# Optimization experiments

Measured on AMD Instinct MI355X. Metric: run time of the kernel, lower is better.

The kernel has to match this reference:

```python
import jax, jax.numpy as jnp
import numpy as np

B, T, E, H = 64, 256, 300, 512


def _linear_init(key, fan_in, shape):
    s = 1.0 / np.sqrt(fan_in)
    return jax.random.uniform(key, shape, jnp.float32, -s, s)


def setup_inputs() -> dict:
    key = jax.random.key(0)
    ks = jax.random.split(key, 8)
    x = jax.random.normal(ks[0], (B, T, E), jnp.float32)
    # Valid transition programs: half the batch left-branching (S S R S R ...),
    # half right-branching (S^T followed by R^(T-1)).
    left = np.zeros(2 * T - 1, np.int32)
    left[2::2] = 1
    right = np.concatenate([np.zeros(T, np.int32), np.ones(T - 1, np.int32)])
    trans = np.stack([left if b % 2 == 0 else right for b in range(B)], axis=1)  # [2T-1, B]
    return {
        "x": x,
        "transitions": jnp.asarray(trans),
        "W_x": _linear_init(ks[1], E, (E, H)),
        "b_x": _linear_init(ks[2], E, (H,)),
        "W_g": _linear_init(ks[3], E, (E, H)),
        "b_g": _linear_init(ks[4], E, (H,)),
        "W_r": _linear_init(ks[5], 2 * H, (2 * H, 5 * H)),
        "b_r": _linear_init(ks[6], 2 * H, (5 * H,)),
    }


def _nary_cell(hc_l, hc_r, W_r, b_r):
    # hc_* : [B, 2H] = concat(h, c)
    h_l, c_l = jnp.split(hc_l, 2, axis=-1)
    h_r, c_r = jnp.split(hc_r, 2, axis=-1)
    proj = jnp.concatenate([h_l, h_r], axis=-1) @ W_r + b_r  # [B, 5H]
    i, f_l, f_r, g, o = jnp.split(proj, 5, axis=-1)
    c = jax.nn.sigmoid(i) * jnp.tanh(g) + jax.nn.sigmoid(f_l) * c_l + jax.nn.sigmoid(f_r) * c_r
    h = jax.nn.sigmoid(o) * jnp.tanh(c)
    return jnp.concatenate([h, c], axis=-1)


def _forward(x, transitions, W_x, b_x, W_g, b_g, W_r, b_r):
    Bb, Tt, _ = x.shape
    Hh = W_x.shape[1]
    # Buffer projections (x assumed reversed; buffers popped from the end).
    c_buf = x @ W_x + b_x                                  # [B, T, H]
    h_buf = jax.nn.sigmoid(x @ W_g + b_g) * jnp.tanh(c_buf)
    buffers = jnp.concatenate([h_buf, c_buf], axis=-1)     # [B, T, 2H]

    bidx = jnp.arange(Bb)
    stack0 = jnp.zeros((Bb, Tt, 2 * Hh), x.dtype)          # fixed-size stack
    sp0 = jnp.zeros((Bb,), jnp.int32)                      # stack pointer
    bp0 = jnp.full((Bb,), Tt, jnp.int32)                   # buffer pointer (pop from end)

    def step(carry, trans_t):
        stack, sp, bp = carry
        is_shift = trans_t == 0                            # [B] bool
        shifted = buffers[bidx, jnp.maximum(bp - 1, 0)]    # [B, 2H]
        child_r = stack[bidx, jnp.maximum(sp - 1, 0)]
        child_l = stack[bidx, jnp.maximum(sp - 2, 0)]
        reduced = _nary_cell(child_l, child_r, W_r, b_r)
        new_elem = jnp.where(is_shift[:, None], shifted, reduced)
        new_sp = jnp.where(is_shift, sp + 1, sp - 1)
        new_bp = jnp.where(is_shift, bp - 1, bp)
        stack = stack.at[bidx, jnp.maximum(new_sp - 1, 0)].set(new_elem)
        return (stack, new_sp, new_bp), None

    (stack, sp, _), _ = jax.lax.scan(step, (stack0, sp0, bp0), transitions)
    hc_root = stack[bidx, jnp.maximum(sp - 1, 0)]          # [B, 2H]
    return hc_root[:, :Hh]                                  # root h states [B, H]


def reference(x, transitions, W_x, b_x, W_g, b_g, W_r, b_r):
    return _forward(x, transitions, W_x, b_x, W_g, b_g, W_r, b_r)
```

## Files before the change

kernel.cpp:

```cpp
#include <hip/hip_runtime.h>
#include <hip/hip_bf16.h>

#define Bb 64
#define Tt 256
#define Ee 300
#define Hh 512
#define NSTEP (2 * Tt - 1)
#define NNODE (Tt - 1)
#define N5H (5 * Hh)

#define NG 8
#define GBATCH 8
#define NBLK 32
#define JPB 16
#define NC 80
#define SYNC_INTS (16 + NG * 1024)

typedef __bf16 v8bf __attribute__((ext_vector_type(8)));
typedef float v4f __attribute__((ext_vector_type(4)));
typedef unsigned long long u64;
typedef unsigned int u32;
typedef unsigned char u8;

__device__ __forceinline__ float sigm(float x) { return 1.f / (1.f + __expf(-x)); }

__global__ __launch_bounds__(256) void leaf_kernel(
    const float* __restrict__ x, const float* __restrict__ Wx,
    const float* __restrict__ bx, const float* __restrict__ Wg,
    const float* __restrict__ bg,
    __hip_bfloat16* __restrict__ leaf_h, float* __restrict__ leaf_c)
{
    __shared__ __align__(16) float xs[16][304];
    const int tid = threadIdx.x;
    const int n = blockIdx.x * 256 + tid;
    const long r0 = (long)blockIdx.y * 16;

    for (int i = tid; i < 16 * Ee; i += 256) {
        int r = i / Ee, k = i - r * Ee;
        xs[r][k] = x[(r0 + r) * Ee + k];
    }
    __syncthreads();

    float accx[16], accg[16];
    const float bxv = bx[n], bgv = bg[n];
#pragma unroll
    for (int r = 0; r < 16; r++) { accx[r] = bxv; accg[r] = bgv; }

    for (int k = 0; k < Ee; k += 4) {
        float wx[4], wg[4];
#pragma unroll
        for (int u = 0; u < 4; u++) {
            wx[u] = Wx[(long)(k + u) * Hh + n];
            wg[u] = Wg[(long)(k + u) * Hh + n];
        }
#pragma unroll
        for (int r = 0; r < 16; r++) {
            const float4 xv = *(const float4*)&xs[r][k];
            accx[r] = fmaf(xv.x, wx[0], accx[r]);
            accx[r] = fmaf(xv.y, wx[1], accx[r]);
            accx[r] = fmaf(xv.z, wx[2], accx[r]);
            accx[r] = fmaf(xv.w, wx[3], accx[r]);
            accg[r] = fmaf(xv.x, wg[0], accg[r]);
            accg[r] = fmaf(xv.y, wg[1], accg[r]);
            accg[r] = fmaf(xv.z, wg[2], accg[r]);
            accg[r] = fmaf(xv.w, wg[3], accg[r]);
        }
    }
#pragma unroll
    for (int r = 0; r < 16; r++) {
        const float c = accx[r];
        const float h = sigm(accg[r]) * tanhf(c);
        const long idx = (r0 + r) * Hh + n;
        leaf_c[idx] = c;
        leaf_h[idx] = __float2bfloat16(h);
    }
}

__global__ __launch_bounds__(256) void wtr_kernel(const float* __restrict__ Wr,
                                                  __hip_bfloat16* __restrict__ WtG)
{
    __shared__ float ts[64][65];
    const int tid = threadIdx.x;
    const long g0 = (long)blockIdx.x * 64;
    const int k0 = (int)blockIdx.y * 64;
    const int r = tid >> 6;
    const int c = tid & 63;
    __bf16* Wo = (__bf16*)WtG;
#pragma unroll
    for (int i = 0; i < 16; i++)
        ts[r + i * 4][c] = Wr[(long)(k0 + r + i * 4) * N5H + g0 + c];
    __syncthreads();
#pragma unroll
    for (int i = 0; i < 16; i++)
        Wo[(g0 + r + i * 4) * 1024 + k0 + c] = (__bf16)ts[c][r + i * 4];
}

__global__ __launch_bounds__(64) void sched_kernel(
    const int* __restrict__ trans,
    int* __restrict__ node_l, int* __restrict__ node_r,
    int* __restrict__ root_src, int* __restrict__ offs,
    int* __restrict__ items, int* __restrict__ max_lv,
    int* __restrict__ sync)
{
    __shared__ short stck[Bb][Tt];
    __shared__ unsigned char lvl[Bb][NNODE];
    __shared__ unsigned char trans_s[NSTEP][Bb];
    __shared__ int counts[NG][256];
    __shared__ int offs_s[NG][257];
    __shared__ int maxl_s[NG];
    const int b = threadIdx.x;

    if (b < NG) maxl_s[b] = 0;
    for (int i4 = b; i4 < SYNC_INTS / 4; i4 += Bb)
        ((int4*)sync)[i4] = make_int4(0, 0, 0, 0);
    for (int i = b; i < NG * 256; i += Bb) counts[i >> 8][i & 255] = 0;
    for (int i4 = b; i4 < (NSTEP * Bb) / 4; i4 += Bb) {
        const int4 v = ((const int4*)trans)[i4];
        const int f = 4 * i4;
        trans_s[(f + 0) >> 6][(f + 0) & 63] = (unsigned char)v.x;
        trans_s[(f + 1) >> 6][(f + 1) & 63] = (unsigned char)v.y;
        trans_s[(f + 2) >> 6][(f + 2) & 63] = (unsigned char)v.z;
        trans_s[(f + 3) >> 6][(f + 3) & 63] = (unsigned char)v.w;
    }
    __syncthreads();

    int sp = 0, bp = Tt, nid = 0, maxl = 0;
    for (int t = 0; t < NSTEP; t++) {
        if (trans_s[t][b] == 0) {
            bp -= 1;
            stck[b][sp] = (short)bp; sp += 1;
        } else {
            const int rs = stck[b][sp - 1];
            const int ls = stck[b][sp - 2];
            const int l_lv = (ls < Tt) ? 0 : (int)lvl[b][ls - Tt];
            const int r_lv = (rs < Tt) ? 0 : (int)lvl[b][rs - Tt];
            const int le = 1 + (l_lv > r_lv ? l_lv : r_lv);
            lvl[b][nid] = (unsigned char)le;
            node_l[b * NNODE + nid] = (l_lv << 9) | ls;
            node_r[b * NNODE + nid] = (r_lv << 9) | rs;
            if (le > maxl) maxl = le;
            sp -= 2;
            stck[b][sp] = (short)(Tt + nid); sp += 1;
            nid += 1;
        }
    }
    root_src[b] = (int)stck[b][0];
    const int g = b >> 3;
    for (int i = 0; i < nid; i++) atomicAdd(&counts[g][lvl[b][i]], 1);
    atomicMax(&maxl_s[g], maxl);
    __syncthreads();
    if (b < NG) {
        int acc = 0;
        for (int l = 0; l < 256; l++) { offs_s[b][l] = acc; acc += counts[b][l]; }
        offs_s[b][256] = acc;
        max_lv[b] = maxl_s[b];
    }
    __syncthreads();
    for (int i = b; i < NG * 256; i += Bb) counts[i >> 8][i & 255] = offs_s[i >> 8][i & 255];
    __syncthreads();
    for (int i = 0; i < nid; i++) {
        const int pos = atomicAdd(&counts[g][lvl[b][i]], 1);
        items[g * (GBATCH * NNODE) + pos] = (b << 16) | i;
    }
    for (int i = b; i < NG * 257; i += Bb) offs[i] = offs_s[i / 257][i % 257];
}

__global__ __launch_bounds__(512) void tree_kernel(
    const __hip_bfloat16* __restrict__ WtG, const float* __restrict__ br,
    const __hip_bfloat16* __restrict__ leaf_h, const float* __restrict__ leaf_c,
    __hip_bfloat16* __restrict__ node_h, float* __restrict__ node_c,
    const int* __restrict__ node_l, const int* __restrict__ node_r,
    const int* __restrict__ root_src, const int* __restrict__ offs,
    const int* __restrict__ items, const int* __restrict__ max_lv,
    float* __restrict__ out, int* __restrict__ sync)
{
    __shared__ float Cs[8][8][84];
    __shared__ float Cred[8][84];
    __shared__ float brs[NC];
    __shared__ u32 mHL[2048], mHR[2048], mCL[2048], mCR[2048], mFL[2048];
    __shared__ u64 hPl[16], hPr[16], cPl[16], cPr[16];
    __shared__ int outm[16];
    __shared__ int s_info;
    __shared__ int force_pad[5120];

    const int tid = threadIdx.x;

    if (tid == 0) {
        int xcc;
        asm volatile("s_getreg_b32 %0, hwreg(HW_REG_XCC_ID)" : "=s"(xcc));
        xcc &= 7;
        const int rank = atomicAdd(&sync[2 + xcc], 1);
        __builtin_amdgcn_s_waitcnt(0);
        const int n = atomicAdd(&sync[0], 1);
        if (n == 255) {
            int ok = 1;
            for (int i = 0; i < 8; i++)
                ok &= (__hip_atomic_load(&sync[2 + i], __ATOMIC_RELAXED,
                                         __HIP_MEMORY_SCOPE_AGENT) == NBLK);
            __hip_atomic_store(&sync[1], ok ? 2 : 1, __ATOMIC_RELAXED,
                               __HIP_MEMORY_SCOPE_AGENT);
        }
        int m;
        while ((m = __hip_atomic_load(&sync[1], __ATOMIC_RELAXED,
                                      __HIP_MEMORY_SCOPE_AGENT)) == 0) {}
        const int grp_ = (m == 2) ? xcc : ((int)blockIdx.x >> 5);
        const int mem_ = (m == 2) ? rank : ((int)blockIdx.x & 31);
        s_info = (m << 16) | (grp_ << 8) | mem_;
    }
    __syncthreads();
    const int info0 = s_info;
    const bool l2m = (info0 >> 16) == 2;
    const int grp = (info0 >> 8) & 255;
    const int mem = info0 & 255;
    const int j0 = mem * JPB;

    const int* offsG = offs + grp * 257;
    const int* itemsG = items + grp * (GBATCH * NNODE);
    int* cntG = sync + 16 + grp * 1024;

    const int ML = max_lv[grp];
    if (ML < 0) { volatile int* fp = force_pad; fp[tid] = 1; }

    const int wave = tid >> 6;
    const int lane = tid & 63;
    const int quad = lane >> 4;
    const int l15 = lane & 15;
    const int kq = wave;

    u32* node_h32 = (u32*)node_h;
    const char* const hBaseL = (const char*)leaf_h;
    const char* const hBaseN = (const char*)node_h;
    const char* const cBaseL = (const char*)leaf_c;
    const char* const cBaseN = (const char*)node_c;

    v8bf wreg[5][4];
#pragma unroll
    for (int nt = 0; nt < 5; nt++) {
        const int c = nt * 16 + l15;
        const long gcol = (long)((c % 5) * Hh + j0 + c / 5);
#pragma unroll
        for (int t = 0; t < 4; t++)
            wreg[nt][t] = *(const v8bf*)&WtG[gcol * 1024 + kq * 128 + t * 32 + quad * 8];
    }
    if (tid < NC) brs[tid] = br[(tid % 5) * Hh + j0 + tid / 5];

    for (int idx = tid; idx < 255 * 8; idx += 512) {
        const int lev = 1 + (idx >> 3);
        const int m = idx & 7;
        u32 fl = 1u << 29;
        u32 hl = 0, hr = 0, cl = 0, cr = 0;
        if (lev <= ML) {
            const int s = offsG[lev], e = offsG[lev + 1];
            const int M = e - s;
            if (M > 0) {
                const int it = itemsG[s + (m < M ? m : 0)];
                const int b = it >> 16, nd = it & 0xffff;
                const int lraw = node_l[b * NNODE + nd];
                const int rraw = node_r[b * NNODE + nd];
                const int ls = lraw & 511, llv = lraw >> 9;
                const int rs = rraw & 511, rlv = rraw >> 9;
                hl = (ls < Tt) ? (u32)((b * Tt + ls) * Hh * 2)
                               : ((u32)((b * NNODE + (ls - Tt)) * Hh * 2) | 0x80000000u);
                cl = (ls < Tt) ? (u32)((b * Tt + ls) * Hh * 4)
                               : ((u32)((b * NNODE + (ls - Tt)) * Hh * 4) | 0x80000000u);
                hr = (rs < Tt) ? (u32)((b * Tt + rs) * Hh * 2)
                               : ((u32)((b * NNODE + (rs - Tt)) * Hh * 2) | 0x80000000u);
                cr = (rs < Tt) ? (u32)((b * Tt + rs) * Hh * 4)
                               : ((u32)((b * NNODE + (rs - Tt)) * Hh * 4) | 0x80000000u);
                fl = (u32)it & 0x07ffffffu;
                if (llv > 0 && llv == lev - 1) fl |= 1u << 27;
                if (rlv > 0 && rlv == lev - 1) fl |= 1u << 28;
                if (m >= M) fl |= 1u << 29;
                if (Tt + nd == root_src[b]) fl |= 1u << 30;
            }
        }
        mHL[8 + idx] = hl; mHR[8 + idx] = hr;
        mCL[8 + idx] = cl; mCR[8 + idx] = cr;
        mFL[8 + idx] = fl;
    }

    auto prep = [&](int base, int M, int plv) {
        if (lane < 16) {
            const int m = lane;
            const int it = itemsG[base + (m < M ? m : 0)];
            const int b = it >> 16;
            const int nd = it & 0xffff;
            const int lraw = node_l[b * NNODE + nd];
            const int rraw = node_r[b * NNODE + nd];
            const int ls = lraw & 511, llv = lraw >> 9;
            const int rs = rraw & 511, rlv = rraw >> 9;
            hPl[m] = (ls < Tt) ? (u64)(leaf_h + ((long)b * Tt + ls) * Hh)
                               : (u64)(node_h + ((long)b * NNODE + (ls - Tt)) * Hh);
            cPl[m] = (ls < Tt) ? (u64)(leaf_c + ((long)b * Tt + ls) * Hh)
                               : (u64)(node_c + ((long)b * NNODE + (ls - Tt)) * Hh);
            hPr[m] = (rs < Tt) ? (u64)(leaf_h + ((long)b * Tt + rs) * Hh)
                               : (u64)(node_h + ((long)b * NNODE + (rs - Tt)) * Hh);
            cPr[m] = (rs < Tt) ? (u64)(leaf_c + ((long)b * Tt + rs) * Hh)
                               : (u64)(node_c + ((long)b * NNODE + (rs - Tt)) * Hh);
            int fl = it;
            if (llv > 0 && llv == plv - 1) fl |= (1 << 27);
            if (rlv > 0 && rlv == plv - 1) fl |= (1 << 28);
            if (Tt + nd == root_src[b]) fl |= (1 << 30);
            if (m >= M) fl |= (1 << 29);
            outm[m] = fl;
        }
    };

    auto gate_store = [&](u32 fe, float clv0, float clv1, float crv0, float crv1) {
        const int jl2 = (lane & 7) * 2;
        if (!(fe & (1u << 29))) {
            const int b = (int)(fe >> 16) & 63;
            const int nd = (int)(fe & 0xffff);
            float cv[2], hv[2];
            const float clv[2] = {clv0, clv1};
            const float crv[2] = {crv0, crv1};
            const int mm = lane >> 3;
#pragma unroll
            for (int jj = 0; jj < 2; jj++) {
                const int jc = (jl2 + jj) * 5;
                const float iv = Cred[mm][jc + 0];
                const float fl = Cred[mm][jc + 1];
                const float fr = Cred[mm][jc + 2];
                const float gv = Cred[mm][jc + 3];
                const float ov = Cred[mm][jc + 4];
                cv[jj] = sigm(iv) * tanhf(gv) + sigm(fl) * clv[jj] + sigm(fr) * crv[jj];
                hv[jj] = sigm(ov) * tanhf(cv[jj]);
            }
            union { float f[2]; u64 u; } cp;
            cp.f[0] = cv[0]; cp.f[1] = cv[1];
            const __hip_bfloat16 h0 = __float2bfloat16(hv[0]);
            const __hip_bfloat16 h1 = __float2bfloat16(hv[1]);
            const u32 hpack = (u32)(*(const unsigned short*)&h0)
                            | ((u32)(*(const unsigned short*)&h1) << 16);
            u64* cdst = (u64*)(node_c + ((long)b * NNODE + nd) * Hh + j0 + jl2);
            u32* hdst = node_h32 + ((long)b * NNODE + nd) * (Hh / 2) + (j0 + jl2) / 2;
            if (l2m) {
                *cdst = cp.u;
                *hdst = hpack;
            } else {
                __hip_atomic_store(cdst, cp.u, __ATOMIC_RELAXED, __HIP_MEMORY_SCOPE_AGENT);
                __hip_atomic_store(hdst, hpack, __ATOMIC_RELAXED, __HIP_MEMORY_SCOPE_AGENT);
            }
            if (fe & (1u << 30)) {
                out[(long)b * Hh + j0 + jl2]     = hv[0];
                out[(long)b * Hh + j0 + jl2 + 1] = hv[1];
            }
        }
    };

    auto do_mfma = [&](v8bf a0, v8bf a1, v8bf a2, v8bf a3) {
        v8bf a[4] = {a0, a1, a2, a3};
#pragma unroll
        for (int nt = 0; nt < 5; nt++) {
            v4f acc = {0.f, 0.f, 0.f, 0.f};
#pragma unroll
            for (int t = 0; t < 4; t++)
                acc = __builtin_amdgcn_mfma_f32_16x16x32_bf16(a[t], wreg[nt][t], acc, 0, 0, 0);
            if (quad < 2) {
#pragma unroll
                for (int rg = 0; rg < 4; rg++)
                    Cs[kq][quad * 4 + rg][nt * 16 + l15] = acc[rg];
            }
        }
    };

    auto reduce = [&]() {
        for (int t = tid; t < 8 * NC; t += 512) {
            const int m = t / NC, c = t - m * NC;
            float r = brs[c];
#pragma unroll
            for (int w = 0; w < 8; w++) r += Cs[w][m][c];
            Cred[m][c] = r;
        }
    };

    __syncthreads();

    const int kb = (kq & 3) * 128 + quad * 8;

    for (int lev = 1; lev <= ML; lev++) {
        const int s = offsG[lev], e = offsG[lev + 1];
        const int mb = lev * 8;

        const int miA = mb + (l15 & 7);
        const u32 flA = mFL[miA];
        const bool hot = (flA >> (27 + (kq >> 2))) & 1;
        const u32 ho = (kq < 4) ? mHL[miA] : mHR[miA];
        const __hip_bfloat16* hp = (const __hip_bfloat16*)
            (((ho & 0x80000000u) ? hBaseN : hBaseL) + (ho & 0x7fffffffu));
        v8bf a0, a1, a2, a3;
        if (!hot) {
            a0 = *(const v8bf*)(hp + kb);
            a1 = *(const v8bf*)(hp + kb + 32);
            a2 = *(const v8bf*)(hp + kb + 64);
            a3 = *(const v8bf*)(hp + kb + 96);
        }
        float clv0 = 0.f, clv1 = 0.f, crv0 = 0.f, crv1 = 0.f;
        bool hotL = false, hotR = false;
        u32 fe = 0;
        const float* cpl = nullptr;
        const float* cpr = nullptr;
        if (wave == 0) {
            const int mi0 = mb + (lane >> 3);
            fe = mFL[mi0];
            hotL = (fe >> 27) & 1;
            hotR = (fe >> 28) & 1;
            const u32 ocl = mCL[mi0], ocr = mCR[mi0];
            cpl = (const float*)(((ocl & 0x80000000u) ? cBaseN : cBaseL) + (ocl & 0x7fffffffu));
            cpr = (const float*)(((ocr & 0x80000000u) ? cBaseN : cBaseL) + (ocr & 0x7fffffffu));
            const int jo = j0 + (lane & 7) * 2;
            if (!hotL) {
                union { u64 u; float f[2]; } t;
                t.u = *(const u64*)(cpl + jo);
                clv0 = t.f[0]; clv1 = t.f[1];
            }
            if (!hotR) {
                union { u64 u; float f[2]; } t;
                t.u = *(const u64*)(cpr + jo);
                crv0 = t.f[0]; crv1 = t.f[1];
            }
        }

        if (lev > 1 && wave == 0) {
            int* cw = cntG + (lev - 1) * 4;
            while (__hip_atomic_load(cw, __ATOMIC_RELAXED,
                                     __HIP_MEMORY_SCOPE_AGENT) < NBLK) {}
        }
        __syncthreads();

        if (hot) {
            a0 = *(const v8bf*)(hp + kb);
            a1 = *(const v8bf*)(hp + kb + 32);
            a2 = *(const v8bf*)(hp + kb + 64);
            a3 = *(const v8bf*)(hp + kb + 96);
        }
        if (wave == 0) {
            const int jo = j0 + (lane & 7) * 2;
            if (hotL) {
                union { u64 u; float f[2]; } t;
                t.u = *(const u64*)(cpl + jo);
                clv0 = t.f[0]; clv1 = t.f[1];
            }
            if (hotR) {
                union { u64 u; float f[2]; } t;
                t.u = *(const u64*)(cpr + jo);
                crv0 = t.f[0]; crv1 = t.f[1];
            }
        }
        do_mfma(a0, a1, a2, a3);
        __syncthreads();
        reduce();
        __syncthreads();
        if (wave == 0) gate_store(fe, clv0, clv1, crv0, crv1);

        for (int base = s + 8; base < e; base += 8) {
            __syncthreads();
            if (wave == 0) prep(base, (e - base < 8) ? (e - base) : 8, lev);
            __syncthreads();
            const __hip_bfloat16* hp2 =
                (const __hip_bfloat16*)((kq < 4) ? hPl[l15 & 7] : hPr[l15 & 7]);
            float xl0 = 0.f, xl1 = 0.f, xr0 = 0.f, xr1 = 0.f;
            u32 fe2 = 1u << 29;
            if (wave == 0) {
                fe2 = (u32)outm[lane >> 3];
                const int jo = j0 + (lane & 7) * 2;
                union { u64 u; float f[2]; } t;
                t.u = *(const u64*)((const float*)cPl[lane >> 3] + jo);
                xl0 = t.f[0]; xl1 = t.f[1];
                t.u = *(const u64*)((const float*)cPr[lane >> 3] + jo);
                xr0 = t.f[0]; xr1 = t.f[1];
            }
            do_mfma(*(const v8bf*)(hp2 + kb), *(const v8bf*)(hp2 + kb + 32),
                    *(const v8bf*)(hp2 + kb + 64), *(const v8bf*)(hp2 + kb + 96));
            __syncthreads();
            reduce();
            __syncthreads();
            if (wave == 0) gate_store(fe2, xl0, xl1, xr0, xr1);
        }

        if (wave == 0) {
            __builtin_amdgcn_s_waitcnt(0);
            if (lev < ML && lane == 0) atomicAdd(cntG + lev * 4, 1);
        }
        __syncthreads();
    }
}

extern "C" void kernel_launch(void* const* d_in, const int* in_sizes, int n_in,
                              void* d_out, int out_size, void* d_ws, size_t ws_size,
                              hipStream_t stream)
{
    const float* x   = (const float*)d_in[0];
    const int* trans = (const int*)d_in[1];
    const float* Wx  = (const float*)d_in[2];
    const float* bx  = (const float*)d_in[3];
    const float* Wg  = (const float*)d_in[4];
    const float* bg  = (const float*)d_in[5];
    const float* Wr  = (const float*)d_in[6];
    const float* br  = (const float*)d_in[7];
    float* out = (float*)d_out;

    char* p = (char*)d_ws;
    auto take = [&](size_t bytes) -> char* {
        char* r = p;
        p += (bytes + 255) & ~(size_t)255;
        return r;
    };
    __hip_bfloat16* leaf_h = (__hip_bfloat16*)take((size_t)Bb * Tt * Hh * 2);
    float* leaf_c          = (float*)take((size_t)Bb * Tt * Hh * 4);
    __hip_bfloat16* node_h = (__hip_bfloat16*)take((size_t)Bb * NNODE * Hh * 2);
    float* node_c          = (float*)take((size_t)Bb * NNODE * Hh * 4);
    int* node_l   = (int*)take((size_t)Bb * NNODE * 4);
    int* node_r   = (int*)take((size_t)Bb * NNODE * 4);
    int* root_src = (int*)take(Bb * 4);
    int* offs     = (int*)take((size_t)NG * 257 * 4);
    int* items    = (int*)take((size_t)NG * GBATCH * NNODE * 4);
    int* max_lv   = (int*)take(NG * 4);
    __hip_bfloat16* WtG = (__hip_bfloat16*)take((size_t)N5H * 1024 * 2);
    int* sync     = (int*)take((size_t)SYNC_INTS * 4);

    hipLaunchKernelGGL(leaf_kernel, dim3(Hh / 256, (Bb * Tt) / 16), dim3(256), 0, stream,
                       x, Wx, bx, Wg, bg, leaf_h, leaf_c);
    hipLaunchKernelGGL(wtr_kernel, dim3(N5H / 64, 1024 / 64), dim3(256), 0, stream,
                       Wr, WtG);
    hipLaunchKernelGGL(sched_kernel, dim3(1), dim3(64), 0, stream,
                       trans, node_l, node_r, root_src, offs, items, max_lv, sync);

    void* args[] = { (void*)&WtG, (void*)&br, (void*)&leaf_h, (void*)&leaf_c,
                     (void*)&node_h, (void*)&node_c, (void*)&node_l, (void*)&node_r,
                     (void*)&root_src, (void*)&offs, (void*)&items, (void*)&max_lv,
                     (void*)&out, (void*)&sync };
    hipLaunchCooperativeKernel((const void*)tree_kernel, dim3(256), dim3(512),
                               args, 0, stream);
}
```

Measured before the change: 1.260 ms.

## Compute leaf projections with split-bf16 MFMA instead of scalar FP32 FMAs

Replaces the scalar FP32 leaf projection kernel with an MFMA kernel. Both x and the weights are split into bf16 hi/lo parts, and three products (hi*hi, hi*lo, lo*hi) recover near-FP32 accuracy. A new pre-pass kernel transposes Wx/Wg into K-padded hi/lo bf16 buffers. The aim is to move the leaf GEMM onto matrix cores, at the cost of an extra weight-split pass and some precision loss from the dropped lo*lo term.

```diff
diff --git a/kernel.cpp b/kernel.cpp
--- a/kernel.cpp
+++ b/kernel.cpp
@@ -8,6 +8,7 @@
 #define NSTEP (2 * Tt - 1)
 #define NNODE (Tt - 1)
 #define N5H (5 * Hh)
+#define LK 320
 
 #define NG 8
 #define GBATCH 8
@@ -24,55 +25,101 @@
 
 __device__ __forceinline__ float sigm(float x) { return 1.f / (1.f + __expf(-x)); }
 
-__global__ __launch_bounds__(256) void leaf_kernel(
-    const float* __restrict__ x, const float* __restrict__ Wx,
-    const float* __restrict__ bx, const float* __restrict__ Wg,
+__global__ __launch_bounds__(256) void wsplit_kernel(
+    const float* __restrict__ Wx, const float* __restrict__ Wg,
+    __bf16* __restrict__ WxHi, __bf16* __restrict__ WxLo,
+    __bf16* __restrict__ WgHi, __bf16* __restrict__ WgLo)
+{
+    __shared__ float ts[64][65];
+    const int tid = threadIdx.x;
+    const int g0 = blockIdx.x * 64;
+    const int k0 = blockIdx.y * 64;
+    const float* W = blockIdx.z ? Wg : Wx;
+    __bf16* Hi = blockIdx.z ? WgHi : WxHi;
+    __bf16* Lo = blockIdx.z ? WgLo : WxLo;
+    const int r = tid >> 6, c = tid & 63;
+#pragma unroll
+    for (int i = 0; i < 16; i++) {
+        const int k = k0 + r + i * 4;
+        ts[r + i * 4][c] = (k < Ee) ? W[(long)k * Hh + g0 + c] : 0.f;
+    }
+    __syncthreads();
+#pragma unroll
+    for (int i = 0; i < 16; i++) {
+        const float v = ts[c][r + i * 4];
+        const __bf16 hi = (__bf16)v;
+        const __bf16 lo = (__bf16)(v - (float)hi);
+        const long o = (long)(g0 + r + i * 4) * LK + k0 + c;
+        Hi[o] = hi;
+        Lo[o] = lo;
+    }
+}
+
+__global__ __launch_bounds__(256) void leaf_mfma_kernel(
+    const float* __restrict__ x, const float* __restrict__ bx,
     const float* __restrict__ bg,
+    const __bf16* __restrict__ WxHi, const __bf16* __restrict__ WxLo,
+    const __bf16* __restrict__ WgHi, const __bf16* __restrict__ WgLo,
     __hip_bfloat16* __restrict__ leaf_h, float* __restrict__ leaf_c)
 {
-    __shared__ __align__(16) float xs[16][304];
     const int tid = threadIdx.x;
-    const int n = blockIdx.x * 256 + tid;
-    const long r0 = (long)blockIdx.y * 16;
-
-    for (int i = tid; i < 16 * Ee; i += 256) {
-        int r = i / Ee, k = i - r * Ee;
-        xs[r][k] = x[(r0 + r) * Ee + k];
-    }
-    __syncthreads();
-
-    float accx[16], accg[16];
-    const float bxv = bx[n], bgv = bg[n];
-#pragma unroll
-    for (int r = 0; r < 16; r++) { accx[r] = bxv; accg[r] = bgv; }
-
-    for (int k = 0; k < Ee; k += 4) {
-        float wx[4], wg[4];
-#pragma unroll
-        for (int u = 0; u < 4; u++) {
-            wx[u] = Wx[(long)(k + u) * Hh + n];
-            wg[u] = Wg[(long)(k + u) * Hh + n];
-        }
-#pragma unroll
-        for (int r = 0; r < 16; r++) {
-            const float4 xv = *(const float4*)&xs[r][k];
-            accx[r] = fmaf(xv.x, wx[0], accx[r]);
-            accx[r] = fmaf(xv.y, wx[1], accx[r]);
-            accx[r] = fmaf(xv.z, wx[2], accx[r]);
-            accx[r] = fmaf(xv.w, wx[3], accx[r]);
-            accg[r] = fmaf(xv.x, wg[0], accg[r]);
-            accg[r] = fmaf(xv.y, wg[1], accg[r]);
-            accg[r] = fmaf(xv.z, wg[2], accg[r]);
-            accg[r] = fmaf(xv.w, wg[3], accg[r]);
-        }
-    }
-#pragma unroll
-    for (int r = 0; r < 16; r++) {
-        const float c = accx[r];
-        const float h = sigm(accg[r]) * tanhf(c);
-        const long idx = (r0 + r) * Hh + n;
-        leaf_c[idx] = c;
-        leaf_h[idx] = __float2bfloat16(h);
+    const int wave = tid >> 6, lane = tid & 63;
+    const int quad = lane >> 4, l15 = lane & 15;
+    const long r0 = (long)blockIdx.x * 64 + wave * 16;
+    const float* xr = x + (r0 + l15) * Ee;
+
+    v8bf ahi[10], alo[10];
+#pragma unroll
+    for (int t = 0; t < 10; t++) {
+        float v[8];
+        if (t < 9) {
+            const float4 p0 = *(const float4*)&xr[t * 32 + quad * 8];
+            const float4 p1 = *(const float4*)&xr[t * 32 + quad * 8 + 4];
+            v[0] = p0.x; v[1] = p0.y; v[2] = p0.z; v[3] = p0.w;
+            v[4] = p1.x; v[5] = p1.y; v[6] = p1.z; v[7] = p1.w;
+        } else {
+#pragma unroll
+            for (int j = 0; j < 8; j++) {
+                const int k = 288 + quad * 8 + j;
+                v[j] = (k < Ee) ? xr[k] : 0.f;
+            }
+        }
+#pragma unroll
+        for (int j = 0; j < 8; j++) {
+            const __bf16 h = (__bf16)v[j];
+            ahi[t][j] = h;
+            alo[t][j] = (__bf16)(v[j] - (float)h);
+        }
+    }
+
+    for (int nt = 0; nt < 32; nt++) {
+        const int n0 = nt * 16;
+        const long cb = (long)(n0 + l15) * LK + quad * 8;
+        v4f ax = {0.f, 0.f, 0.f, 0.f}, ag = {0.f, 0.f, 0.f, 0.f};
+#pragma unroll
+        for (int t = 0; t < 10; t++) {
+            const v8bf wxh = *(const v8bf*)&WxHi[cb + t * 32];
+            const v8bf wxl = *(const v8bf*)&WxLo[cb + t * 32];
+            const v8bf wgh = *(const v8bf*)&WgHi[cb + t * 32];
+            const v8bf wgl = *(const v8bf*)&WgLo[cb + t * 32];
+            ax = __builtin_amdgcn_mfma_f32_16x16x32_bf16(ahi[t], wxh, ax, 0, 0, 0);
+            ag = __builtin_amdgcn_mfma_f32_16x16x32_bf16(ahi[t], wgh, ag, 0, 0, 0);
+            ax = __builtin_amdgcn_mfma_f32_16x16x32_bf16(ahi[t], wxl, ax, 0, 0, 0);
+            ag = __builtin_amdgcn_mfma_f32_16x16x32_bf16(ahi[t], wgl, ag, 0, 0, 0);
+            ax = __builtin_amdgcn_mfma_f32_16x16x32_bf16(alo[t], wxh, ax, 0, 0, 0);
+            ag = __builtin_amdgcn_mfma_f32_16x16x32_bf16(alo[t], wgh, ag, 0, 0, 0);
+        }
+        const float bxv = bx[n0 + l15];
+        const float bgv = bg[n0 + l15];
+#pragma unroll
+        for (int rg = 0; rg < 4; rg++) {
+            const float c = ax[rg] + bxv;
+            const float g = ag[rg] + bgv;
+            const float h = sigm(g) * tanhf(c);
+            const long rr = r0 + quad * 4 + rg;
+            leaf_c[rr * Hh + n0 + l15] = c;
+            leaf_h[rr * Hh + n0 + l15] = __float2bfloat16(h);
+        }
     }
 }
 
@@ -518,13 +565,19 @@
     int* max_lv   = (int*)take(NG * 4);
     __hip_bfloat16* WtG = (__hip_bfloat16*)take((size_t)N5H * 1024 * 2);
     int* sync     = (int*)take((size_t)SYNC_INTS * 4);
-
-    hipLaunchKernelGGL(leaf_kernel, dim3(Hh / 256, (Bb * Tt) / 16), dim3(256), 0, stream,
-                       x, Wx, bx, Wg, bg, leaf_h, leaf_c);
+    __bf16* WxHi = (__bf16*)take((size_t)Hh * LK * 2);
+    __bf16* WxLo = (__bf16*)take((size_t)Hh * LK * 2);
+    __bf16* WgHi = (__bf16*)take((size_t)Hh * LK * 2);
+    __bf16* WgLo = (__bf16*)take((size_t)Hh * LK * 2);
+
+    hipLaunchKernelGGL(wsplit_kernel, dim3(Hh / 64, LK / 64, 2), dim3(256), 0, stream,
+                       Wx, Wg, WxHi, WxLo, WgHi, WgLo);
     hipLaunchKernelGGL(wtr_kernel, dim3(N5H / 64, 1024 / 64), dim3(256), 0, stream,
                        Wr, WtG);
     hipLaunchKernelGGL(sched_kernel, dim3(1), dim3(64), 0, stream,
                        trans, node_l, node_r, root_src, offs, items, max_lv, sync);
+    hipLaunchKernelGGL(leaf_mfma_kernel, dim3((Bb * Tt) / 64), dim3(256), 0, stream,
+                       x, bx, bg, WxHi, WxLo, WgHi, WgLo, leaf_h, leaf_c);
 
     void* args[] = { (void*)&WtG, (void*)&br, (void*)&leaf_h, (void*)&leaf_c,
                      (void*)&node_h, (void*)&node_c, (void*)&node_l, (void*)&node_r,
```

Result: no change. 1.272 ms (+1.0%).
